# Kernel optimization log

Measured on AMD Instinct MI355X. Metric: run time of the kernel, lower is better.

Reference implementation:

```python
import jax, jax.numpy as jnp
import numpy as np
from jax import lax

sg = lax.stop_gradient

# (kernel, stride, pad, pool_k, pool_s) for the 7 conv blocks
CFG = [(16, 2, 7, 8, 4), (12, 2, 5, 4, 2), (9, 1, 4, 5, 2), (7, 1, 3, 4, 2),
       (5, 1, 2, 2, 2), (3, 1, 1, 2, 2), (3, 1, 1, 2, 2)]
W_SHAPES = [(8, 1, 16), (12, 8, 12), (32, 12, 9), (64, 32, 7),
            (64, 64, 5), (64, 64, 3), (72, 64, 3)]
CH = [8, 12, 32, 64, 64, 64, 72]


def bin_act(x):
    # forward: sign(x); backward: clipped-quadratic surrogate (STE)
    s = jnp.sign(x)
    le = (x < -1.0).astype(x.dtype)
    ri = (x >= 1.0).astype(x.dtype)
    cl = ((x >= -1.0) & (x < 0.0)).astype(x.dtype)
    cr = ((x >= 0.0) & (x < 1.0)).astype(x.dtype)
    out = cl * (2.0 + x) * x + cr * (2.0 - x) * x + ri - le
    return sg(s) + out - sg(out)


def bin_wei(w, axes):
    # forward: scale * sign(w) with scale = mean|w| (detached); backward through tanh (STE)
    scale = sg(jnp.mean(jnp.abs(w), axis=axes, keepdims=True))
    t = jnp.tanh(w)
    return sg(scale * jnp.sign(w)) + t - sg(t)


def conv1d(x, w, stride, pad):
    return lax.conv_general_dilated(x, w, (stride,), [(pad, pad)],
                                    dimension_numbers=('NCH', 'OIH', 'NCH'))


def maxpool1d(x, k, s):
    return lax.reduce_window(x, -jnp.inf, lax.max, (1, 1, k), (1, 1, s), 'VALID')


def batchnorm1d(x, gamma, beta, eps=1e-5):
    # training-mode BN: batch statistics over (N, L), biased variance
    m = jnp.mean(x, axis=(0, 2), keepdims=True)
    v = jnp.mean((x - m) ** 2, axis=(0, 2), keepdims=True)
    return gamma[None, :, None] * (x - m) / jnp.sqrt(v + eps) + beta[None, :, None]


def _forward(x, ws, gs, bs, wfc):
    for w, g, b, (k, s, p, pk, ps) in zip(ws, gs, bs, CFG):
        x = conv1d(x, bin_wei(w, (1, 2)), s, p)
        x = maxpool1d(x, pk, ps)
        x = batchnorm1d(x, g, b)
        x = bin_act(x)
    x = x.reshape(x.shape[0], -1)                 # [B, 72*3]
    return x @ bin_wei(wfc, (1,)).T               # [B, classCount]


def setup_inputs() -> dict:
    key = jax.random.key(0)
    ks = jax.random.split(key, 9)
    inp = {'x': jax.random.normal(ks[0], (2048, 1, 3600), dtype=jnp.float32)}
    for i, shp in enumerate(W_SHAPES):
        inp[f'w{i+1}'] = jax.random.uniform(ks[i + 1], shp, dtype=jnp.float32) * 0.32
        inp[f'g{i+1}'] = jnp.ones((CH[i],), jnp.float32)
        inp[f'b{i+1}'] = jnp.zeros((CH[i],), jnp.float32)
    inp['wfc'] = jax.random.uniform(ks[8], (5, 216), dtype=jnp.float32) * 0.32
    return inp


def reference(x, w1, w2, w3, w4, w5, w6, w7,
              g1, g2, g3, g4, g5, g6, g7,
              b1, b2, b3, b4, b5, b6, b7, wfc):
    ws = [w1, w2, w3, w4, w5, w6, w7]
    gs = [g1, g2, g3, g4, g5, g6, g7]
    bs = [b1, b2, b3, b4, b5, b6, b7]
    return _forward(x, ws, gs, bs, wfc)
```

## Files before the change

kernel.cpp:

```cpp
#include <hip/hip_runtime.h>
#include <math.h>
#include <stdint.h>

#define NBATCH 2048
#define NSLOT 32

struct Args {
    const float* x;
    const float* W[7];
    const float* G[7];
    const float* Bt[7];
    const float* WFC;
    float* out;
    float* bufA;
    float* bufB;
    double* stats;
    float* wsc;
    uint32_t* wmb;
};

__device__ __forceinline__ float signf(float v) {
    return (v > 0.f) ? 1.f : ((v < 0.f) ? -1.f : 0.f);
}

__global__ __launch_bounds__(256) void k_setup(Args a) {
    const int blk = blockIdx.x, tid = threadIdx.x;
    for (int i = blk * 256 + tid; i < NSLOT * 632; i += 391 * 256) a.stats[i] = 0.0;

    if (blk < 321 && tid < 64) {
        const int cum[9] = {0,8,20,52,116,180,244,316,321};
        const int per[8] = {16,96,108,224,320,192,192,216};
        const float* wsrc[8] = {a.W[0],a.W[1],a.W[2],a.W[3],a.W[4],a.W[5],a.W[6],a.WFC};
        int o = blk, L = 0;
        while (L < 7 && o >= cum[L + 1]) ++L;
        const int oo = o - cum[L], p = per[L];
        const float* wo = wsrc[L] + (size_t)oo * p;
        float s = 0.f;
        for (int i = tid; i < p; i += 64) s += fabsf(wo[i]);
        #pragma unroll
        for (int off = 32; off; off >>= 1) s += __shfl_down(s, off);
        if (tid == 0) a.wsc[o] = s / (float)p;
    }

    const int gid = (blk - 384) * 256 + tid;
    if (blk >= 384 && gid >= 0 && gid < 1608) {
        const int cum[7]  = {0,144,432,880,1200,1392,1608};
        const int cin[6]  = {8,12,32,64,64,64};
        const int kk[6]   = {12,9,7,5,3,3};
        const int wpp[6]  = {1,1,1,2,2,2};
        const int woff[6] = {0,144,432,880,1520,1904};
        const float* wsrc[6] = {a.W[1],a.W[2],a.W[3],a.W[4],a.W[5],a.W[6]};
        int L = 0;
        while (L < 5 && gid >= cum[L + 1]) ++L;
        const int idx = gid - cum[L];
        const int K = kk[L], CIN = cin[L], WPP = wpp[L];
        const int o = idx / K, k = idx - o * K;
        const float* w = wsrc[L];
        uint32_t m0 = 0, m1 = 0;
        for (int c = 0; c < CIN; ++c) {
            const float v = w[((size_t)o * CIN + c) * K + k];
            const uint32_t bit = (v < 0.f) ? 1u : 0u;
            int bp = c;
            if (CIN == 64) bp = 16 * (c & 3) + (c >> 2);
            else if (CIN == 32) bp = 8 * (c & 3) + (c >> 2);
            if (bp < 32) m0 |= bit << bp; else m1 |= bit << (bp - 32);
        }
        uint32_t* dst = a.wmb + woff[L] + (size_t)idx * WPP;
        dst[0] = m0;
        if (WPP == 2) dst[1] = m1;
    }
}

__global__ __launch_bounds__(256) void k_conv1(Args a) {
    __shared__ float wgs[128];
    __shared__ double sred[16];
    const int n = blockIdx.x, tid = threadIdx.x, l = tid & 63;
    if (tid < 128) wgs[tid] = signf(a.W[0][tid]);
    if (tid < 16)  sred[tid] = 0.0;
    __syncthreads();
    const int r = tid;
    const float* xn = a.x + (size_t)n * 3600;
    float m0[8], m1[8];
    #pragma unroll
    for (int ch = 0; ch < 8; ++ch) { m0[ch] = 0.f; m1[ch] = 0.f; }
    if (r < 225) {
        float f[40];
        const int g0 = 16 * r - 8;
        #pragma unroll
        for (int b = 0; b < 10; ++b) {
            const int gg = g0 + 4 * b;
            if (gg >= 0 && gg <= 3596) {
                const float4 v = *(const float4*)(xn + gg);
                f[4*b] = v.x; f[4*b+1] = v.y; f[4*b+2] = v.z; f[4*b+3] = v.w;
            } else {
                f[4*b] = 0.f; f[4*b+1] = 0.f; f[4*b+2] = 0.f; f[4*b+3] = 0.f;
            }
        }
        #pragma unroll
        for (int ch = 0; ch < 8; ++ch) {
            float acc[12];
            #pragma unroll
            for (int j = 0; j < 12; ++j) acc[j] = 0.f;
            #pragma unroll
            for (int k = 0; k < 16; ++k) {
                const float wk = wgs[ch * 16 + k];
                #pragma unroll
                for (int j = 0; j < 12; ++j)
                    acc[j] = fmaf(f[2*j + 1 + k], wk, acc[j]);
            }
            const float lo  = fmaxf(fmaxf(acc[0], acc[1]), fmaxf(acc[2], acc[3]));
            const float mid = fmaxf(fmaxf(acc[4], acc[5]), fmaxf(acc[6], acc[7]));
            const float hi  = fmaxf(fmaxf(acc[8], acc[9]), fmaxf(acc[10], acc[11]));
            const float sc = a.wsc[ch];
            m0[ch] = fmaxf(lo, mid) * sc;
            m1[ch] = (r < 224) ? fmaxf(mid, hi) * sc : 0.f;
        }
        float* on = a.bufA + ((size_t)n * 449 + 2 * r) * 8;
        *(float4*)(on + 0) = make_float4(m0[0], m0[1], m0[2], m0[3]);
        *(float4*)(on + 4) = make_float4(m0[4], m0[5], m0[6], m0[7]);
        if (r < 224) {
            *(float4*)(on + 8)  = make_float4(m1[0], m1[1], m1[2], m1[3]);
            *(float4*)(on + 12) = make_float4(m1[4], m1[5], m1[6], m1[7]);
        }
    }
    #pragma unroll
    for (int ch = 0; ch < 8; ++ch) {
        double sS = (double)m0[ch] + (double)m1[ch];
        double s2 = (double)m0[ch] * m0[ch] + (double)m1[ch] * m1[ch];
        #pragma unroll
        for (int off = 32; off; off >>= 1) {
            sS += __shfl_down(sS, off);
            s2 += __shfl_down(s2, off);
        }
        if (l == 0) {
            atomicAdd(&sred[ch], sS);
            atomicAdd(&sred[8 + ch], s2);
        }
    }
    __syncthreads();
    if (tid < 16) {
        double* so = a.stats + (size_t)(n & (NSLOT - 1)) * 16;
        atomicAdd(&so[tid], sred[tid]);
    }
}

template <int CIN, int LIN, int O, int K, int STRIDE, int PAD,
          int PK, int PS, int LP, int WPP, int LPB, bool SF64>
__device__ __forceinline__ void bin_body(
    const float* __restrict__ xprev, const uint32_t* __restrict__ wm,
    const float* __restrict__ wsc, const float* __restrict__ wsc_prev,
    const double* __restrict__ stats_in,
    const float* __restrict__ gamma, const float* __restrict__ beta,
    const double cntInv, float* __restrict__ out, double* __restrict__ stats_out)
{
    constexpr int OL    = (O < 64) ? O : 64;
    constexpr int PO    = 64 / OL;
    constexpr int SPAN  = (PK - 1) * STRIDE + K;
    constexpr int SHIFT = (WPP == 1) ? (PAD & 1) : 0;
    constexpr int QSPAN = 4 * LPB * PS * STRIDE + SPAN + 2;
    constexpr int XM64A = (WPP == 2) ? QSPAN : ((QSPAN + 3) / 2 + 1);
    constexpr int F     = 2 * CIN;
    constexpr int FW    = (F > 64) ? 128 : 64;

    __shared__ uint64_t xmbuf[XM64A];
    __shared__ long long foldU[4][FW];
    __shared__ int sS[4][O], sS2[4][O];

    const int tid = threadIdx.x;
    const int wv  = tid >> 6;
    const int l   = tid & 63;
    uint32_t* xm32 = (uint32_t*)xmbuf;
    uint64_t* xm64 = xmbuf;

    const int n    = blockIdx.x;
    const int lp0b = blockIdx.y * (4 * LPB);
    const int lp1b = (lp0b + 4 * LPB < LP) ? lp0b + 4 * LPB : LP;
    const int q0raw = lp0b * PS * STRIDE - PAD;
    const int q0 = (q0raw > 0) ? q0raw : 0;
    const int q1raw = (lp1b - 1) * PS * STRIDE - PAD + SPAN;
    const int q1 = (q1raw < LIN) ? q1raw : LIN;
    const int S0 = (WPP == 1) ? ((q0 + SHIFT) & 1) : 0;
    const int xbase = q0 - S0;

    const int lp0 = lp0b + wv * LPB;
    const int lp1 = (lp0 + LPB < lp1b) ? lp0 + LPB : lp1b;

    const float* xn = xprev + (size_t)n * LIN * CIN;

    {
        const long long* stI = (const long long*)stats_in;
        long long pa = 0, pb_ = 0;
        double da = 0.0;
        #pragma unroll
        for (int s8 = 0; s8 < 8; ++s8) {
            const int s = (wv << 3) + s8;
            if constexpr (SF64) {
                if (l < F) da += stats_in[s * F + l];
            } else {
                if (l < ((F < 64) ? F : 64)) pa += stI[s * F + l];
                if constexpr (F > 64) { if (l < F - 64) pb_ += stI[s * F + 64 + l]; }
            }
        }
        if constexpr (SF64) foldU[wv][l] = __double_as_longlong(da);
        else {
            foldU[wv][l] = pa;
            if constexpr (F > 64) foldU[wv][64 + l] = pb_;
        }
    }
    __syncthreads();
    float aA = 0.f, aB = 0.f;
    {
        double t0 = 0.0, t1 = 0.0;
        if constexpr (SF64) {
            double tot = 0.0;
            #pragma unroll
            for (int w = 0; w < 4; ++w) tot += __longlong_as_double(foldU[w][l]);
            t0 = tot;
            t1 = __shfl(tot, CIN + l);
        } else if constexpr (F > 64) {
            long long a0 = 0, a1 = 0;
            #pragma unroll
            for (int w = 0; w < 4; ++w) { a0 += foldU[w][l]; a1 += foldU[w][64 + l]; }
            t0 = (double)a0; t1 = (double)a1;
        } else {
            long long a0 = 0;
            #pragma unroll
            for (int w = 0; w < 4; ++w) a0 += foldU[w][l];
            const double tot = (double)a0;
            t0 = tot;
            t1 = __shfl(tot, CIN + l);
        }
        if (l < CIN) {
            double mean, E2;
            if constexpr (SF64) { mean = t0 * cntInv; E2 = t1 * cntInv; }
            else {
                const double w = (double)wsc_prev[l];
                mean = w * t0 * cntInv; E2 = w * w * t1 * cntInv;
            }
            const double var = E2 - mean * mean;
            const double inv = 1.0 / sqrt(var + 1e-5);
            const double av  = (double)gamma[l] * inv;
            aA = (float)av;
            aB = (float)((double)beta[l] - mean * av);
        }
    }

    if constexpr (CIN == 64) {
        const int sub = l & 15, grp = l >> 4;
        const float a0 = __shfl(aA, 4*sub),     b0 = __shfl(aB, 4*sub);
        const float a1 = __shfl(aA, 4*sub + 1), b1 = __shfl(aB, 4*sub + 1);
        const float a2 = __shfl(aA, 4*sub + 2), b2 = __shfl(aB, 4*sub + 2);
        const float a3 = __shfl(aA, 4*sub + 3), b3 = __shfl(aB, 4*sub + 3);
        for (int pb = q0 + wv * 4; pb < q1; pb += 16) {
            const int pos = pb + grp;
            const bool valid = pos < q1;
            const float4 v = *(const float4*)(xn + (size_t)(valid ? pos : q0) * 64 + 4*sub);
            const unsigned long long bal0 = __ballot(valid && (fmaf(a0, v.x, b0) < 0.f));
            const unsigned long long bal1 = __ballot(valid && (fmaf(a1, v.y, b1) < 0.f));
            const unsigned long long bal2 = __ballot(valid && (fmaf(a2, v.z, b2) < 0.f));
            const unsigned long long bal3 = __ballot(valid && (fmaf(a3, v.w, b3) < 0.f));
            if (l < 4 && pb + l < q1) {
                const uint64_t m = ((bal0 >> (16*l)) & 0xFFFFull)
                                 | (((bal1 >> (16*l)) & 0xFFFFull) << 16)
                                 | (((bal2 >> (16*l)) & 0xFFFFull) << 32)
                                 | (((bal3 >> (16*l)) & 0xFFFFull) << 48);
                xm64[pb + l - xbase] = m;
            }
        }
    } else if constexpr (CIN == 32) {
        const int sub = l & 7, grp = l >> 3;
        const float a0 = __shfl(aA, 4*sub),     b0 = __shfl(aB, 4*sub);
        const float a1 = __shfl(aA, 4*sub + 1), b1 = __shfl(aB, 4*sub + 1);
        const float a2 = __shfl(aA, 4*sub + 2), b2 = __shfl(aB, 4*sub + 2);
        const float a3 = __shfl(aA, 4*sub + 3), b3 = __shfl(aB, 4*sub + 3);
        for (int pb = q0 + wv * 8; pb < q1; pb += 32) {
            const int pos = pb + grp;
            const bool valid = pos < q1;
            const float4 v = *(const float4*)(xn + (size_t)(valid ? pos : q0) * 32 + 4*sub);
            const unsigned long long bal0 = __ballot(valid && (fmaf(a0, v.x, b0) < 0.f));
            const unsigned long long bal1 = __ballot(valid && (fmaf(a1, v.y, b1) < 0.f));
            const unsigned long long bal2 = __ballot(valid && (fmaf(a2, v.z, b2) < 0.f));
            const unsigned long long bal3 = __ballot(valid && (fmaf(a3, v.w, b3) < 0.f));
            if (l < 8 && pb + l < q1) {
                const uint32_t m = (uint32_t)((bal0 >> (8*l)) & 0xFFull)
                                 | ((uint32_t)((bal1 >> (8*l)) & 0xFFull) << 8)
                                 | ((uint32_t)((bal2 >> (8*l)) & 0xFFull) << 16)
                                 | ((uint32_t)((bal3 >> (8*l)) & 0xFFull) << 24);
                xm32[pb + l - xbase] = m;
            }
        }
    } else if constexpr (CIN == 8) {
        const int sub = l & 1, grp = l >> 1;
        const float a0 = __shfl(aA, 4*sub),     b0 = __shfl(aB, 4*sub);
        const float a1 = __shfl(aA, 4*sub + 1), b1 = __shfl(aB, 4*sub + 1);
        const float a2 = __shfl(aA, 4*sub + 2), b2 = __shfl(aB, 4*sub + 2);
        const float a3 = __shfl(aA, 4*sub + 3), b3 = __shfl(aB, 4*sub + 3);
        for (int pb = q0 + wv * 32; pb < q1; pb += 128) {
            const int pos = pb + grp;
            const bool valid = pos < q1;
            const float4 v = *(const float4*)(xn + (size_t)(valid ? pos : q0) * 8 + 4*sub);
            const unsigned long long bal0 = __ballot(valid && (fmaf(a0, v.x, b0) < 0.f));
            const unsigned long long bal1 = __ballot(valid && (fmaf(a1, v.y, b1) < 0.f));
            const unsigned long long bal2 = __ballot(valid && (fmaf(a2, v.z, b2) < 0.f));
            const unsigned long long bal3 = __ballot(valid && (fmaf(a3, v.w, b3) < 0.f));
            if (l < 32 && pb + l < q1) {
                const uint32_t t0 = (uint32_t)((bal0 >> (2*l)) & 3ull);
                const uint32_t t1 = (uint32_t)((bal1 >> (2*l)) & 3ull);
                const uint32_t t2 = (uint32_t)((bal2 >> (2*l)) & 3ull);
                const uint32_t t3 = (uint32_t)((bal3 >> (2*l)) & 3ull);
                const uint32_t m = (t0 & 1) | ((t1 & 1) << 1) | ((t2 & 1) << 2) | ((t3 & 1) << 3)
                                 | ((t0 >> 1) << 4) | ((t1 >> 1) << 5) | ((t2 >> 1) << 6) | ((t3 >> 1) << 7);
                xm32[pb + l - xbase] = m;
            }
        }
    } else {
        constexpr int PPW = 64 / CIN;
        const int pw = l / CIN, c = l - pw * CIN;
        const float myA = __shfl(aA, c), myB = __shfl(aB, c);
        const bool lact = (pw < PPW);
        for (int pb = q0 + wv * PPW; pb < q1; pb += 4 * PPW) {
            const int pos = pb + pw;
            const bool act = lact && (pos < q1);
            float v = 0.f;
            if (act) v = fmaf(myA, xn[(size_t)pb * CIN + l], myB);
            const unsigned long long bal = __ballot(act && (v < 0.f));
            if (act && c == 0) {
                const uint32_t mk = (uint32_t)((bal >> (pw * CIN)) & ((1u << CIN) - 1));
                xm32[pos - xbase] = mk;
            }
        }
    }
    __syncthreads();

    float* on = out + (size_t)n * LP * O;

    if constexpr (WPP == 2) {
        const uint64_t* wmp = (const uint64_t*)wm;
        uint64_t wr[K];
        #pragma unroll
        for (int k = 0; k < K; ++k) wr[k] = wmp[l * K + k];
        uint64_t wr2[K];
        const int oo2 = 64 + ((O > 64 && l < O - 64) ? l : 0);
        if constexpr (O > 64) {
            #pragma unroll
            for (int k = 0; k < K; ++k) wr2[k] = wmp[oo2 * K + k];
        }
        const float myws  = wsc[l];
        const float myws2 = (O > 64 && l < O - 64) ? wsc[64 + l] : 0.f;
        int accS = 0, accS2 = 0, accSb = 0, accS2b = 0;

        for (int lp = lp0; lp < lp1; ++lp) {
            const int lo = lp * PS * STRIDE - PAD;
            int m = -1000000, m2 = -1000000;
            if (lo >= 0 && lo + SPAN <= LIN) {
                uint64_t tw[SPAN];
                #pragma unroll
                for (int t = 0; t < SPAN; ++t) tw[t] = xm64[lo - xbase + t];
                #pragma unroll
                for (int j = 0; j < PK; ++j) {
                    int p = 0;
                    #pragma unroll
                    for (int k = 0; k < K; ++k)
                        p += __popcll(tw[j * STRIDE + k] ^ wr[k]);
                    m = max(m, CIN * K - 2 * p);
                    if constexpr (O > 64) {
                        int p2 = 0;
                        #pragma unroll
                        for (int k = 0; k < K; ++k)
                            p2 += __popcll(tw[j * STRIDE + k] ^ wr2[k]);
                        m2 = max(m2, CIN * K - 2 * p2);
                    }
                }
            } else {
                #pragma unroll
                for (int j = 0; j < PK; ++j) {
                    const int base = lo + j * STRIDE;
                    int p = 0, nv = 0, p2 = 0;
                    #pragma unroll
                    for (int k = 0; k < K; ++k) {
                        const int q = base + k;
                        if (q >= 0 && q < LIN) {
                            ++nv;
                            const uint64_t xv = xm64[q - xbase];
                            p += __popcll(xv ^ wr[k]);
                            if constexpr (O > 64) p2 += __popcll(xv ^ wr2[k]);
                        }
                    }
                    m = max(m, CIN * nv - 2 * p);
                    if constexpr (O > 64) m2 = max(m2, CIN * nv - 2 * p2);
                }
            }
            on[lp * O + l] = (float)m * myws;
            accS += m; accS2 += m * m;
            if constexpr (O > 64) {
                if (l < O - 64) {
                    on[lp * O + 64 + l] = (float)m2 * myws2;
                    accSb += m2; accS2b += m2 * m2;
                }
            }
        }
        sS[wv][l] = accS; sS2[wv][l] = accS2;
        if constexpr (O > 64) {
            if (l < O - 64) { sS[wv][64 + l] = accSb; sS2[wv][64 + l] = accS2b; }
        }
    } else {
        const int po = l / OL, oo = l - po * OL;
        const bool cact = (po < PO);
        const float myws = cact ? wsc[oo] : 0.f;
        uint32_t wr[K];
        #pragma unroll
        for (int k = 0; k < K; ++k) wr[k] = wm[(cact ? oo : 0) * K + k];
        int accS = 0, accS2 = 0;

        constexpr int PAIRS = (SPAN + 1) / 2;
        for (int lp = lp0 + po; lp < lp1; lp += PO) {
            const int lo = lp * PS * STRIDE - PAD;
            int m = -1000000;
            if (lo >= 0 && lo + SPAN <= LIN) {
                uint32_t tw[PAIRS * 2];
                const int e0 = (lo - xbase) >> 1;
                #pragma unroll
                for (int i = 0; i < PAIRS; ++i) {
                    const uint64_t u = xm64[e0 + i];
                    tw[2 * i]     = (uint32_t)u;
                    tw[2 * i + 1] = (uint32_t)(u >> 32);
                }
                #pragma unroll
                for (int j = 0; j < PK; ++j) {
                    int p = 0;
                    #pragma unroll
                    for (int k = 0; k < K; ++k)
                        p += __popc(tw[j * STRIDE + k] ^ wr[k]);
                    m = max(m, CIN * K - 2 * p);
                }
            } else {
                #pragma unroll
                for (int j = 0; j < PK; ++j) {
                    const int base = lo + j * STRIDE;
                    int p = 0, nv = 0;
                    #pragma unroll
                    for (int k = 0; k < K; ++k) {
                        const int q = base + k;
                        if (q >= 0 && q < LIN) { ++nv; p += __popc(xm32[q - xbase] ^ wr[k]); }
                    }
                    m = max(m, CIN * nv - 2 * p);
                }
            }
            if (cact) {
                on[lp * O + oo] = (float)m * myws;
                accS += m; accS2 += m * m;
            }
        }
        int t = accS, t2 = accS2;
        #pragma unroll
        for (int g = 1; g < PO; ++g) {
            t  += __shfl(accS,  l + g * OL);
            t2 += __shfl(accS2, l + g * OL);
        }
        if (l < OL) { sS[wv][l] = t; sS2[wv][l] = t2; }
    }
    __syncthreads();

    unsigned long long* soU =
        (unsigned long long*)stats_out + (size_t)(n & (NSLOT - 1)) * 2 * O;
    for (int t = tid; t < 2 * O; t += 256) {
        int tot;
        if (t < O) tot = sS[0][t] + sS[1][t] + sS[2][t] + sS[3][t];
        else { const int f = t - O; tot = sS2[0][f] + sS2[1][f] + sS2[2][f] + sS2[3][f]; }
        atomicAdd(&soU[t], (unsigned long long)(long long)tot);
    }
}

#define BIN_PARAMS \
    const float* __restrict__ xprev, const uint32_t* __restrict__ wm, \
    const float* __restrict__ wsc, const float* __restrict__ wsc_prev, \
    const double* __restrict__ stats_in, \
    const float* __restrict__ gamma, const float* __restrict__ beta, \
    const double cntInv, float* __restrict__ out, double* __restrict__ stats_out
#define BIN_ARGS xprev, wm, wsc, wsc_prev, stats_in, gamma, beta, cntInv, out, stats_out

__global__ __launch_bounds__(256) void k_bin2(BIN_PARAMS) { bin_body< 8,449,12,12,2,5,4,2,111,1,14,true >(BIN_ARGS); }
__global__ __launch_bounds__(256) void k_bin3(BIN_PARAMS) { bin_body<12,111,32, 9,1,4,5,2, 54,1,14,false>(BIN_ARGS); }
__global__ __launch_bounds__(256) void k_bin4(BIN_PARAMS) { bin_body<32, 54,64, 7,1,3,4,2, 26,1, 7,false>(BIN_ARGS); }
__global__ __launch_bounds__(256) void k_bin5(BIN_PARAMS) { bin_body<64, 26,64, 5,1,2,2,2, 13,2, 4,false>(BIN_ARGS); }
__global__ __launch_bounds__(256) void k_bin6(BIN_PARAMS) { bin_body<64, 13,64, 3,1,1,2,2,  6,2, 2,false>(BIN_ARGS); }
__global__ __launch_bounds__(256) void k_bin7(BIN_PARAMS) { bin_body<64,  6,72, 3,1,1,2,2,  3,2, 1,false>(BIN_ARGS); }

__global__ __launch_bounds__(256) void k_fc(Args a) {
    const int n = blockIdx.x * 4 + (int)(threadIdx.x >> 6);
    const int l = (int)(threadIdx.x & 63);
    const long long* st = (const long long*)(a.stats + 15616);
    long long s = 0, s2 = 0, sb = 0, s2b = 0;
    #pragma unroll 4
    for (int sl = 0; sl < NSLOT; ++sl) {
        s  += st[sl * 144 + l];
        s2 += st[sl * 144 + 72 + l];
        if (l < 8) {
            sb  += st[sl * 144 + 64 + l];
            s2b += st[sl * 144 + 72 + 64 + l];
        }
    }
    float aA0, aB0, aA1 = 0.f, aB1 = 0.f;
    {
        const double w = (double)a.wsc[244 + l];
        const double mean = w * (double)s / 6144.0;
        const double E2   = w * w * (double)s2 / 6144.0;
        const double var  = E2 - mean * mean;
        const double inv  = 1.0 / sqrt(var + 1e-5);
        const double aa   = (double)a.G[6][l] * inv;
        aA0 = (float)aa; aB0 = (float)((double)a.Bt[6][l] - mean * aa);
    }
    if (l < 8) {
        const double w = (double)a.wsc[244 + 64 + l];
        const double mean = w * (double)sb / 6144.0;
        const double E2   = w * w * (double)s2b / 6144.0;
        const double var  = E2 - mean * mean;
        const double inv  = 1.0 / sqrt(var + 1e-5);
        const double aa   = (double)a.G[6][64 + l] * inv;
        aA1 = (float)aa; aB1 = (float)((double)a.Bt[6][64 + l] - mean * aa);
    }
    const float* p7 = a.bufA + (size_t)n * 216;
    float acc[5] = {0.f, 0.f, 0.f, 0.f, 0.f};
    #pragma unroll
    for (int j = 0; j < 4; ++j) {
        const int i = l + 64 * j;
        const int ic = (i < 216) ? i : 215;
        const int c = ic / 3, lp = ic - 3 * c;
        float aa = __shfl(aA0, c);
        float bb = __shfl(aB0, c);
        const float aaH = __shfl(aA1, c - 64);
        const float bbH = __shfl(aB1, c - 64);
        if (c >= 64) { aa = aaH; bb = bbH; }
        if (i < 216) {
            const float av = signf(fmaf(aa, p7[lp * 72 + c], bb));
            #pragma unroll
            for (int o = 0; o < 5; ++o)
                acc[o] += av * signf(a.WFC[o * 216 + i]);
        }
    }
    #pragma unroll
    for (int o = 0; o < 5; ++o) {
        float v = acc[o];
        #pragma unroll
        for (int off = 32; off; off >>= 1) v += __shfl_down(v, off);
        if (l == 0) a.out[(size_t)n * 5 + o] = v * a.wsc[316 + o];
    }
}

extern "C" void kernel_launch(void* const* d_in, const int* in_sizes, int n_in,
                              void* d_out, int out_size, void* d_ws, size_t ws_size,
                              hipStream_t stream) {
    Args a;
    a.x = (const float*)d_in[0];
    for (int i = 0; i < 7; ++i) {
        a.W[i]  = (const float*)d_in[1 + 3 * i];
        a.G[i]  = (const float*)d_in[2 + 3 * i];
        a.Bt[i] = (const float*)d_in[3 + 3 * i];
    }
    a.WFC = (const float*)d_in[22];
    a.out = (float*)d_out;

    char* ws = (char*)d_ws;
    a.bufA  = (float*)ws;
    a.bufB  = (float*)(ws + 29425664);
    a.stats = (double*)(ws + 43057152);
    a.wsc   = (float*)(ws + 43218944);
    a.wmb   = (uint32_t*)d_out;

    k_setup<<<391, 256, 0, stream>>>(a);
    k_conv1<<<NBATCH, 256, 0, stream>>>(a);
    k_bin2<<<dim3(NBATCH, 2), 256, 0, stream>>>(
        a.bufA, a.wmb + 0, a.wsc + 8, a.wsc, a.stats + 0, a.G[0], a.Bt[0],
        1.0/919552.0, a.bufB, a.stats + 512);
    k_bin3<<<dim3(NBATCH, 1), 256, 0, stream>>>(
        a.bufB, a.wmb + 144, a.wsc + 20, a.wsc + 8, a.stats + 512, a.G[1], a.Bt[1],
        1.0/227328.0, a.bufA, a.stats + 1280);
    k_bin4<<<dim3(NBATCH, 1), 256, 0, stream>>>(
        a.bufA, a.wmb + 432, a.wsc + 52, a.wsc + 20, a.stats + 1280, a.G[2], a.Bt[2],
        1.0/110592.0, a.bufB, a.stats + 3328);
    k_bin5<<<dim3(NBATCH, 1), 256, 0, stream>>>(
        a.bufB, a.wmb + 880, a.wsc + 116, a.wsc + 52, a.stats + 3328, a.G[3], a.Bt[3],
        1.0/53248.0, a.bufA, a.stats + 7424);
    k_bin6<<<dim3(NBATCH, 1), 256, 0, stream>>>(
        a.bufA, a.wmb + 1520, a.wsc + 180, a.wsc + 116, a.stats + 7424, a.G[4], a.Bt[4],
        1.0/26624.0, a.bufB, a.stats + 11520);
    k_bin7<<<dim3(NBATCH, 1), 256, 0, stream>>>(
        a.bufB, a.wmb + 1904, a.wsc + 244, a.wsc + 180, a.stats + 11520, a.G[5], a.Bt[5],
        1.0/12288.0, a.bufA, a.stats + 15616);
    k_fc<<<NBATCH / 4, 256, 0, stream>>>(a);
}
```

Baseline: 272.6 us.

## Pack layer-2/3 binary activations densely as bytes/halfwords for fewer popcounts

For the CIN=8 and CIN=12 binary conv layers, activation bitmasks are now stored as packed uint8/uint16 in shared memory instead of one 32-bit word per position. The weight masks are repacked to match, four taps per word for CIN=8 and with even/odd alignment phases for CIN=12. Each pooled window then needs only 3 or 5 popcounts instead of 12 or 9, and the shared-memory footprint shrinks. The cost is byte-shift extraction logic and new weight-offset bookkeeping that is more fragile to get right.

New measurement: 260.9 us. -4.3%, faster.

```diff
diff --git a/kernel.cpp b/kernel.cpp
--- a/kernel.cpp
+++ b/kernel.cpp
@@ -43,15 +43,15 @@
     }
 
     const int gid = (blk - 384) * 256 + tid;
-    if (blk >= 384 && gid >= 0 && gid < 1608) {
-        const int cum[7]  = {0,144,432,880,1200,1392,1608};
-        const int cin[6]  = {8,12,32,64,64,64};
-        const int kk[6]   = {12,9,7,5,3,3};
-        const int wpp[6]  = {1,1,1,2,2,2};
-        const int woff[6] = {0,144,432,880,1520,1904};
-        const float* wsrc[6] = {a.W[1],a.W[2],a.W[3],a.W[4],a.W[5],a.W[6]};
+    if (blk >= 384 && blk <= 388 && gid >= 0 && gid < 1176) {
+        const int cum[5]  = {0,448,768,960,1176};
+        const int cin[4]  = {32,64,64,64};
+        const int kk[4]   = {7,5,3,3};
+        const int wpp[4]  = {1,2,2,2};
+        const int woff[4] = {356,804,1444,1828};
+        const float* wsrc[4] = {a.W[3],a.W[4],a.W[5],a.W[6]};
         int L = 0;
-        while (L < 5 && gid >= cum[L + 1]) ++L;
+        while (L < 3 && gid >= cum[L + 1]) ++L;
         const int idx = gid - cum[L];
         const int K = kk[L], CIN = cin[L], WPP = wpp[L];
         const int o = idx / K, k = idx - o * K;
@@ -68,6 +68,45 @@
         uint32_t* dst = a.wmb + woff[L] + (size_t)idx * WPP;
         dst[0] = m0;
         if (WPP == 2) dst[1] = m1;
+    }
+
+    if (blk == 389 && tid < 12) {
+        const float* w = a.W[1];
+        const int o = tid;
+        #pragma unroll
+        for (int g = 0; g < 3; ++g) {
+            uint32_t word = 0;
+            #pragma unroll
+            for (int j = 0; j < 4; ++j) {
+                const int k = 4 * g + j;
+                uint32_t by = 0;
+                #pragma unroll
+                for (int c = 0; c < 8; ++c)
+                    by |= (w[((size_t)o * 8 + c) * 12 + k] < 0.f ? 1u : 0u) << c;
+                word |= by << (8 * j);
+            }
+            a.wmb[o * 3 + g] = word;
+        }
+    }
+    if (blk == 390 && tid < 64) {
+        const float* w = a.W[2];
+        const int o = tid >> 1, ph = tid & 1;
+        uint32_t mk[9];
+        #pragma unroll
+        for (int k = 0; k < 9; ++k) {
+            uint32_t m = 0;
+            #pragma unroll
+            for (int c = 0; c < 12; ++c)
+                m |= (w[((size_t)o * 12 + c) * 9 + k] < 0.f ? 1u : 0u) << c;
+            mk[k] = m;
+        }
+        uint32_t wd[5];
+        if (ph == 0) { wd[0]=mk[0]|(mk[1]<<16); wd[1]=mk[2]|(mk[3]<<16);
+                       wd[2]=mk[4]|(mk[5]<<16); wd[3]=mk[6]|(mk[7]<<16); wd[4]=mk[8]; }
+        else         { wd[0]=mk[0]<<16; wd[1]=mk[1]|(mk[2]<<16);
+                       wd[2]=mk[3]|(mk[4]<<16); wd[3]=mk[5]|(mk[6]<<16); wd[4]=mk[7]|(mk[8]<<16); }
+        #pragma unroll
+        for (int g = 0; g < 5; ++g) a.wmb[36 + o * 10 + ph * 5 + g] = wd[g];
     }
 }
 
@@ -156,9 +195,12 @@
     constexpr int OL    = (O < 64) ? O : 64;
     constexpr int PO    = 64 / OL;
     constexpr int SPAN  = (PK - 1) * STRIDE + K;
-    constexpr int SHIFT = (WPP == 1) ? (PAD & 1) : 0;
-    constexpr int QSPAN = 4 * LPB * PS * STRIDE + SPAN + 2;
-    constexpr int XM64A = (WPP == 2) ? QSPAN : ((QSPAN + 3) / 2 + 1);
+    constexpr int QLEN  = 4 * LPB * PS * STRIDE + SPAN;
+    constexpr int XM64A =
+        (WPP == 2)   ? (QLEN + 2)
+      : (CIN == 8)   ? ((QLEN + 48) + 7) / 8
+      : (CIN == 12)  ? ((2 * (QLEN + 10)) + 7) / 8
+      : ((QLEN + 2 + 3) / 2 + 1);
     constexpr int F     = 2 * CIN;
     constexpr int FW    = (F > 64) ? 128 : 64;
 
@@ -171,6 +213,8 @@
     const int l   = tid & 63;
     uint32_t* xm32 = (uint32_t*)xmbuf;
     uint64_t* xm64 = xmbuf;
+    uint16_t* xm16 = (uint16_t*)xmbuf;
+    uint8_t*  xm8  = (uint8_t*)xmbuf;
 
     const int n    = blockIdx.x;
     const int lp0b = blockIdx.y * (4 * LPB);
@@ -179,8 +223,11 @@
     const int q0 = (q0raw > 0) ? q0raw : 0;
     const int q1raw = (lp1b - 1) * PS * STRIDE - PAD + SPAN;
     const int q1 = (q1raw < LIN) ? q1raw : LIN;
-    const int S0 = (WPP == 1) ? ((q0 + SHIFT) & 1) : 0;
-    const int xbase = q0 - S0;
+    int xbase;
+    if constexpr (CIN == 8)       xbase = q0 & ~3;
+    else if constexpr (CIN == 12) xbase = q0 - (q0 & 1);
+    else if constexpr (WPP == 1)  xbase = q0 - ((q0 + (PAD & 1)) & 1);
+    else                          xbase = q0;
 
     const int lp0 = lp0b + wv * LPB;
     const int lp1 = (lp0 + LPB < lp1b) ? lp0 + LPB : lp1b;
@@ -310,7 +357,7 @@
                 const uint32_t t3 = (uint32_t)((bal3 >> (2*l)) & 3ull);
                 const uint32_t m = (t0 & 1) | ((t1 & 1) << 1) | ((t2 & 1) << 2) | ((t3 & 1) << 3)
                                  | ((t0 >> 1) << 4) | ((t1 >> 1) << 5) | ((t2 >> 1) << 6) | ((t3 >> 1) << 7);
-                xm32[pb + l - xbase] = m;
+                xm8[pb + l - xbase] = (uint8_t)m;
             }
         }
     } else {
@@ -326,7 +373,7 @@
             const unsigned long long bal = __ballot(act && (v < 0.f));
             if (act && c == 0) {
                 const uint32_t mk = (uint32_t)((bal >> (pw * CIN)) & ((1u << CIN) - 1));
-                xm32[pos - xbase] = mk;
+                xm16[pos - xbase] = (uint16_t)mk;
             }
         }
     }
@@ -403,6 +450,131 @@
         if constexpr (O > 64) {
             if (l < O - 64) { sS[wv][64 + l] = accSb; sS2[wv][64 + l] = accS2b; }
         }
+    } else if constexpr (CIN == 8) {
+        const int po = l / OL, oo = l - po * OL;
+        const bool cact = (po < PO);
+        const float myws = cact ? wsc[oo] : 0.f;
+        const int osel = cact ? oo : 0;
+        const uint32_t wr0 = wm[osel*3], wr1 = wm[osel*3+1], wr2 = wm[osel*3+2];
+        uint32_t wb[12];
+        #pragma unroll
+        for (int k = 0; k < 12; ++k)
+            wb[k] = ((k < 4 ? wr0 : (k < 8 ? wr1 : wr2)) >> (8 * (k & 3))) & 255u;
+        const uint32_t* xw = (const uint32_t*)xmbuf;
+        int accS = 0, accS2 = 0;
+
+        for (int lp = lp0 + po; lp < lp1; lp += PO) {
+            const int lo = lp * PS * STRIDE - PAD;
+            int m = -1000000;
+            if (lo >= 0 && lo + SPAN <= LIN) {
+                const int bb = lo - xbase;
+                const int w0 = bb >> 2;
+                uint32_t tw[6];
+                #pragma unroll
+                for (int i = 0; i < 6; ++i) tw[i] = xw[w0 + i];
+                #pragma unroll
+                for (int j = 0; j < PK; ++j) {
+                    const int wo = (j + 1) >> 1;
+                    uint32_t e0, e1, e2;
+                    if (j & 1) {
+                        e0 = (tw[wo]   >> 8) | (tw[wo+1] << 24);
+                        e1 = (tw[wo+1] >> 8) | (tw[wo+2] << 24);
+                        e2 = (tw[wo+2] >> 8) | (tw[wo+3] << 24);
+                    } else {
+                        e0 = (tw[wo]   >> 24) | (tw[wo+1] << 8);
+                        e1 = (tw[wo+1] >> 24) | (tw[wo+2] << 8);
+                        e2 = (tw[wo+2] >> 24) | (tw[wo+3] << 8);
+                    }
+                    const int p = __popc(e0 ^ wr0) + __popc(e1 ^ wr1) + __popc(e2 ^ wr2);
+                    m = max(m, 96 - 2 * p);
+                }
+            } else {
+                #pragma unroll
+                for (int j = 0; j < PK; ++j) {
+                    const int base = lo + j * STRIDE;
+                    int p = 0, nv = 0;
+                    #pragma unroll
+                    for (int k = 0; k < 12; ++k) {
+                        const int q = base + k;
+                        if (q >= 0 && q < LIN) { ++nv; p += __popc((uint32_t)xm8[q - xbase] ^ wb[k]); }
+                    }
+                    m = max(m, 8 * nv - 2 * p);
+                }
+            }
+            if (cact) {
+                on[lp * O + oo] = (float)m * myws;
+                accS += m; accS2 += m * m;
+            }
+        }
+        int t = accS, t2 = accS2;
+        #pragma unroll
+        for (int g = 1; g < PO; ++g) {
+            t  += __shfl(accS,  l + g * OL);
+            t2 += __shfl(accS2, l + g * OL);
+        }
+        if (l < OL) { sS[wv][l] = t; sS2[wv][l] = t2; }
+    } else if constexpr (CIN == 12) {
+        const int po = l / OL, oo = l - po * OL;
+        const bool cact = (po < PO);
+        const float myws = cact ? wsc[oo] : 0.f;
+        const int osel = cact ? oo : 0;
+        uint32_t wE[5], wO[5];
+        #pragma unroll
+        for (int g = 0; g < 5; ++g) { wE[g] = wm[osel*10 + g]; wO[g] = wm[osel*10 + 5 + g]; }
+        uint32_t we16[9];
+        we16[0]=wE[0]&0xFFFFu; we16[1]=wE[0]>>16; we16[2]=wE[1]&0xFFFFu; we16[3]=wE[1]>>16;
+        we16[4]=wE[2]&0xFFFFu; we16[5]=wE[2]>>16; we16[6]=wE[3]&0xFFFFu; we16[7]=wE[3]>>16;
+        we16[8]=wE[4]&0xFFFFu;
+        const uint32_t* xw = (const uint32_t*)xmbuf;
+        int accS = 0, accS2 = 0;
+
+        for (int lp = lp0 + po; lp < lp1; lp += PO) {
+            const int lo = lp * PS * STRIDE - PAD;
+            int m = -1000000;
+            if (lo >= 0 && lo + SPAN <= LIN) {
+                const int s0 = (lo - xbase) >> 1;
+                uint32_t tw[7];
+                #pragma unroll
+                for (int i = 0; i < 7; ++i) tw[i] = xw[s0 + i];
+                #pragma unroll
+                for (int j = 0; j < PK; ++j) {
+                    const int o_ = j >> 1;
+                    int p;
+                    if (j & 1)
+                        p = __popc((tw[o_] & 0xFFFF0000u) ^ wO[0]) + __popc(tw[o_+1] ^ wO[1])
+                          + __popc(tw[o_+2] ^ wO[2]) + __popc(tw[o_+3] ^ wO[3])
+                          + __popc(tw[o_+4] ^ wO[4]);
+                    else
+                        p = __popc(tw[o_] ^ wE[0]) + __popc(tw[o_+1] ^ wE[1])
+                          + __popc(tw[o_+2] ^ wE[2]) + __popc(tw[o_+3] ^ wE[3])
+                          + __popc((tw[o_+4] & 0xFFFFu) ^ wE[4]);
+                    m = max(m, 108 - 2 * p);
+                }
+            } else {
+                #pragma unroll
+                for (int j = 0; j < PK; ++j) {
+                    const int base = lo + j * STRIDE;
+                    int p = 0, nv = 0;
+                    #pragma unroll
+                    for (int k = 0; k < 9; ++k) {
+                        const int q = base + k;
+                        if (q >= 0 && q < LIN) { ++nv; p += __popc((uint32_t)xm16[q - xbase] ^ we16[k]); }
+                    }
+                    m = max(m, 12 * nv - 2 * p);
+                }
+            }
+            if (cact) {
+                on[lp * O + oo] = (float)m * myws;
+                accS += m; accS2 += m * m;
+            }
+        }
+        int t = accS, t2 = accS2;
+        #pragma unroll
+        for (int g = 1; g < PO; ++g) {
+            t  += __shfl(accS,  l + g * OL);
+            t2 += __shfl(accS2, l + g * OL);
+        }
+        if (l < OL) { sS[wv][l] = t; sS2[wv][l] = t2; }
     } else {
         const int po = l / OL, oo = l - po * OL;
         const bool cact = (po < PO);
@@ -421,9 +593,9 @@
                 const int e0 = (lo - xbase) >> 1;
                 #pragma unroll
                 for (int i = 0; i < PAIRS; ++i) {
-                    const uint64_t u = xm64[e0 + i];
-                    tw[2 * i]     = (uint32_t)u;
-                    tw[2 * i + 1] = (uint32_t)(u >> 32);
+                    const uint64_t u64v = xm64[e0 + i];
+                    tw[2 * i]     = (uint32_t)u64v;
+                    tw[2 * i + 1] = (uint32_t)(u64v >> 32);
                 }
                 #pragma unroll
                 for (int j = 0; j < PK; ++j) {
@@ -573,19 +745,19 @@
         a.bufA, a.wmb + 0, a.wsc + 8, a.wsc, a.stats + 0, a.G[0], a.Bt[0],
         1.0/919552.0, a.bufB, a.stats + 512);
     k_bin3<<<dim3(NBATCH, 1), 256, 0, stream>>>(
-        a.bufB, a.wmb + 144, a.wsc + 20, a.wsc + 8, a.stats + 512, a.G[1], a.Bt[1],
+        a.bufB, a.wmb + 36, a.wsc + 20, a.wsc + 8, a.stats + 512, a.G[1], a.Bt[1],
         1.0/227328.0, a.bufA, a.stats + 1280);
     k_bin4<<<dim3(NBATCH, 1), 256, 0, stream>>>(
-        a.bufA, a.wmb + 432, a.wsc + 52, a.wsc + 20, a.stats + 1280, a.G[2], a.Bt[2],
+        a.bufA, a.wmb + 356, a.wsc + 52, a.wsc + 20, a.stats + 1280, a.G[2], a.Bt[2],
         1.0/110592.0, a.bufB, a.stats + 3328);
     k_bin5<<<dim3(NBATCH, 1), 256, 0, stream>>>(
-        a.bufB, a.wmb + 880, a.wsc + 116, a.wsc + 52, a.stats + 3328, a.G[3], a.Bt[3],
+        a.bufB, a.wmb + 804, a.wsc + 116, a.wsc + 52, a.stats + 3328, a.G[3], a.Bt[3],
         1.0/53248.0, a.bufA, a.stats + 7424);
     k_bin6<<<dim3(NBATCH, 1), 256, 0, stream>>>(
-        a.bufA, a.wmb + 1520, a.wsc + 180, a.wsc + 116, a.stats + 7424, a.G[4], a.Bt[4],
+        a.bufA, a.wmb + 1444, a.wsc + 180, a.wsc + 116, a.stats + 7424, a.G[4], a.Bt[4],
         1.0/26624.0, a.bufB, a.stats + 11520);
     k_bin7<<<dim3(NBATCH, 1), 256, 0, stream>>>(
-        a.bufB, a.wmb + 1904, a.wsc + 244, a.wsc + 180, a.stats + 11520, a.G[5], a.Bt[5],
+        a.bufB, a.wmb + 1828, a.wsc + 244, a.wsc + 180, a.stats + 11520, a.G[5], a.Bt[5],
         1.0/12288.0, a.bufA, a.stats + 15616);
     k_fc<<<NBATCH / 4, 256, 0, stream>>>(a);
 }
```
